# Kernel tuning notes

Measured on AMD Instinct MI355X. Metric: run time of the kernel, lower is better.

Reference implementation:

```python
import jax, jax.numpy as jnp
import numpy as np

D_MODEL = 1024
N_HEADS = 16
D_HEAD = D_MODEL // N_HEADS
EPS_LN = 1e-5
EPS_GATE = 1e-5
EPS_DEN = 1e-5


def setup_inputs() -> dict:
    key = jax.random.key(0)
    ks = jax.random.split(key, 4)
    B, T, D = 1, 2048, D_MODEL
    x = jax.random.normal(ks[0], (B, T, D), dtype=jnp.float32)
    # Linear weights scaled like torch default init (~1/sqrt(fan_in))
    s = 1.0 / np.sqrt(D)
    qkv_w = jax.random.normal(ks[1], (3 * D, D), dtype=jnp.float32) * s
    gate_w = jax.random.normal(ks[2], (D, D), dtype=jnp.float32) * s
    proj_w = jax.random.normal(ks[3], (D, D), dtype=jnp.float32) * s
    return {
        "x": x,
        "ln_g": jnp.ones((D,), jnp.float32),
        "ln_b": jnp.zeros((D,), jnp.float32),
        "qkv_w": qkv_w,
        "qkv_b": jnp.zeros((3 * D,), jnp.float32),
        "gate_w": gate_w,
        "gate_b": jnp.zeros((D,), jnp.float32),
        "proj_w": proj_w,
        "proj_b": jnp.zeros((D,), jnp.float32),
    }


def _linear(x, w, b):
    # torch nn.Linear: y = x @ W^T + b, W is (out, in)
    return jnp.einsum("btd,od->bto", x, w) + b


def reference(x, ln_g, ln_b, qkv_w, qkv_b, gate_w, gate_b, proj_w, proj_b):
    B, T, D = x.shape
    H, Dh = N_HEADS, D_HEAD

    # LayerNorm
    mu = jnp.mean(x, axis=-1, keepdims=True)
    var = jnp.mean((x - mu) ** 2, axis=-1, keepdims=True)
    x_norm = (x - mu) / jnp.sqrt(var + EPS_LN) * ln_g + ln_b

    qkv = _linear(x_norm, qkv_w, qkv_b)
    q, k, v = jnp.split(qkv, 3, axis=-1)

    # concept gate on raw x
    gate_sig = jax.nn.sigmoid(_linear(x, gate_w, gate_b))
    gate_norm = gate_sig / (jnp.mean(gate_sig, axis=-1, keepdims=True) + EPS_GATE)
    q = q * gate_norm
    k = k * gate_norm

    # (B,T,D) -> (B,H,T,Dh)
    def heads(t):
        return t.reshape(B, T, H, Dh).transpose(0, 2, 1, 3)

    q, k, v = heads(q).astype(jnp.float32), heads(k).astype(jnp.float32), heads(v).astype(jnp.float32)

    q = jax.nn.elu(q) + 1.0
    k = jax.nn.elu(k) + 1.0

    # causal linear attention via cumsum of outer products (same math as source)
    kv = jnp.einsum("bhtd,bhtm->bhtdm", k, v)        # (B,H,T,Dh,Dh)
    kv_cum = jnp.cumsum(kv, axis=2)
    out_num = jnp.einsum("bhtd,bhtdm->bhtm", q, kv_cum)
    k_cum = jnp.cumsum(k, axis=2)
    out_den = jnp.einsum("bhtd,bhtd->bht", q, k_cum)[..., None] + EPS_DEN
    out = out_num / out_den                           # (B,H,T,Dh)

    out = out.astype(x_norm.dtype).transpose(0, 2, 1, 3).reshape(B, T, D)
    return _linear(out, proj_w, proj_b)
```

## Files before the change

kernel.cpp:

```cpp
#include <hip/hip_runtime.h>
#include <hip/hip_bf16.h>
#include <math.h>

#define T_SEQ 2048
#define DM 1024
#define NH 16
#define DH 64
#define CHUNK 64
#define NCHUNK (T_SEQ / CHUNK)

typedef __hip_bfloat16 bf16;
typedef __attribute__((ext_vector_type(8))) short short8;
typedef __attribute__((ext_vector_type(4))) short short4v;
typedef __attribute__((ext_vector_type(4))) float f32x4;

static __device__ __forceinline__ short f2b_bits(float f) {
  bf16 t = __float2bfloat16(f);
  short s;
  __builtin_memcpy(&s, &t, 2);
  return s;
}
static __device__ __forceinline__ float b2f(short s) {
  unsigned int u = ((unsigned int)(unsigned short)s) << 16;
  float f;
  __builtin_memcpy(&f, &u, 4);
  return f;
}
static __device__ __forceinline__ float gelu1(float raw, float gate, float inv) {
  float x = raw * gate * inv;
  return x > 0.f ? x + 1.f : __expf(x);
}
static __device__ __forceinline__ void gload16(const void* g, void* l) {
  __builtin_amdgcn_global_load_lds((const __attribute__((address_space(1))) void*)g,
                                   (__attribute__((address_space(3))) void*)l, 16, 0, 0);
}

#define PREP_WBLOCKS (5 * DM * DM / 4 / 256)
__global__ __launch_bounds__(256) void prep_kernel(
    const float* __restrict__ x, const float* __restrict__ g,
    const float* __restrict__ b, const float* __restrict__ qkv_w,
    const float* __restrict__ gate_w, const float* __restrict__ proj_w,
    bf16* __restrict__ xn, bf16* __restrict__ xbf,
    bf16* __restrict__ wqkv, bf16* __restrict__ wgate, bf16* __restrict__ wproj,
    float* __restrict__ gate_accum) {
  const int blk = blockIdx.x;
  if (blk < T_SEQ) {
    const int row = blk;
    if (row < 8) gate_accum[row * 256 + threadIdx.x] = 0.f;
    const float* xr = x + (size_t)row * DM;
    float vals[4];
    float s = 0.f, s2 = 0.f;
#pragma unroll
    for (int i = 0; i < 4; i++) {
      float v = xr[threadIdx.x + i * 256];
      vals[i] = v;
      s += v;
      s2 += v * v;
    }
#pragma unroll
    for (int m = 1; m < 64; m <<= 1) {
      s += __shfl_xor(s, m, 64);
      s2 += __shfl_xor(s2, m, 64);
    }
    __shared__ float red[8];
    const int wid = threadIdx.x >> 6;
    if ((threadIdx.x & 63) == 0) {
      red[wid] = s;
      red[4 + wid] = s2;
    }
    __syncthreads();
    s = red[0] + red[1] + red[2] + red[3];
    s2 = red[4] + red[5] + red[6] + red[7];
    const float mean = s * (1.f / DM);
    const float var = s2 * (1.f / DM) - mean * mean;
    const float rstd = rsqrtf(var + 1e-5f);
#pragma unroll
    for (int i = 0; i < 4; i++) {
      int idx = threadIdx.x + i * 256;
      float v = (vals[i] - mean) * rstd * g[idx] + b[idx];
      xn[(size_t)row * DM + idx] = __float2bfloat16(v);
      xbf[(size_t)row * DM + idx] = __float2bfloat16(vals[i]);
    }
  } else {
    constexpr int NQ = 3 * DM * DM / 4, NS = DM * DM / 4;
    int i = (blk - T_SEQ) * 256 + threadIdx.x;
    const float* src;
    bf16* dst;
    int j;
    if (i < NQ) { src = qkv_w; dst = wqkv; j = i; }
    else if (i < NQ + NS) { src = gate_w; dst = wgate; j = i - NQ; }
    else { src = proj_w; dst = wproj; j = i - NQ - NS; }
    float4 v = ((const float4*)src)[j];
    short4v sv;
    sv.x = f2b_bits(v.x); sv.y = f2b_bits(v.y); sv.z = f2b_bits(v.z); sv.w = f2b_bits(v.w);
    *(short4v*)&dst[j * 4] = sv;
  }
}

__global__ __launch_bounds__(256) void gemm_gateqkv(
    const bf16* __restrict__ xbf, const bf16* __restrict__ xn,
    const bf16* __restrict__ wg, const bf16* __restrict__ wq,
    const float* __restrict__ gate_b, const float* __restrict__ qkv_b,
    short* __restrict__ Gb, float* __restrict__ gate_accum,
    short* __restrict__ Qb, short* __restrict__ Kb, short* __restrict__ Vb,
    short* __restrict__ VbT) {
  constexpr int K = 1024;
  __shared__ __align__(16) short As[2 * 64 * 32];
  __shared__ __align__(16) short Bs[2 * 128 * 32];

  const int tid = threadIdx.x;
  const int wid = tid >> 6, lane = tid & 63;
  const int wm = wid >> 1, wn = wid & 1;
  const int lm = lane & 15, quad = lane >> 4;

  const int nt = blockIdx.x;
  const bool isGate = nt < 8;
  const int m0 = blockIdx.y * 64;
  const int n0 = (isGate ? nt : nt - 8) * 128;
  const short* Ag = (const short*)(isGate ? xbf : xn);
  const short* Wg = (const short*)(isGate ? wg : wq);

  f32x4 zero = {0.f, 0.f, 0.f, 0.f};
  f32x4 acc[2][4];
#pragma unroll
  for (int i = 0; i < 2; i++)
#pragma unroll
    for (int j = 0; j < 4; j++) acc[i][j] = zero;

  for (int kb = 0; kb < K; kb += 64) {
    __syncthreads();
#pragma unroll
    for (int sec = 0; sec < 2; sec++) {
      {
        const int row = tid >> 2, seg = (tid & 3) * 8;
        gload16(&Ag[(size_t)(m0 + row) * K + kb + sec * 32 + seg],
                &As[sec * 2048 + wid * 512]);
      }
#pragma unroll
      for (int it = 0; it < 2; it++) {
        const int idx = it * 256 + tid;
        const int row = idx >> 2, seg = (idx & 3) * 8;
        gload16(&Wg[(size_t)(n0 + row) * K + kb + sec * 32 + seg],
                &Bs[sec * 4096 + (it * 256 + wid * 64) * 8]);
      }
    }
    __syncthreads();
#pragma unroll
    for (int sec = 0; sec < 2; sec++) {
      short8 afr[2], bfr[4];
#pragma unroll
      for (int i = 0; i < 2; i++)
        afr[i] = *(const short8*)&As[sec * 2048 + (wm * 32 + i * 16 + lm) * 32 + quad * 8];
#pragma unroll
      for (int j = 0; j < 4; j++)
        bfr[j] = *(const short8*)&Bs[sec * 4096 + (wn * 64 + j * 16 + lm) * 32 + quad * 8];
#pragma unroll
      for (int i = 0; i < 2; i++)
#pragma unroll
        for (int j = 0; j < 4; j++)
          acc[i][j] = __builtin_amdgcn_mfma_f32_16x16x32_bf16(afr[i], bfr[j], acc[i][j], 0, 0, 0);
    }
  }

  if (isGate) {
    float* red = (float*)As;
    __syncthreads();
#pragma unroll
    for (int i = 0; i < 2; i++) {
#pragma unroll
      for (int r = 0; r < 4; r++) {
        const int rowl = wm * 32 + i * 16 + quad * 4 + r;
        const int row = m0 + rowl;
        float rp = 0.f;
#pragma unroll
        for (int j = 0; j < 4; j++) {
          const int col = n0 + wn * 64 + j * 16 + lm;
          float v = acc[i][j][r] + gate_b[col];
          float sig = 1.f / (1.f + __expf(-v));
          Gb[(size_t)row * DM + col] = f2b_bits(sig);
          rp += sig;
        }
        red[rowl * 32 + wn * 16 + lm] = rp;
      }
    }
    __syncthreads();
    if (tid < 64) {
      float s = 0.f;
#pragma unroll
      for (int t2 = 0; t2 < 32; t2++) s += red[tid * 32 + t2];
      atomicAdd(&gate_accum[m0 + tid], s);
    }
  } else {
#pragma unroll
    for (int i = 0; i < 2; i++) {
      const int rbase = m0 + wm * 32 + i * 16 + quad * 4;
#pragma unroll
      for (int j = 0; j < 4; j++) {
        const int col = n0 + wn * 64 + j * 16 + lm;
        const float bval = qkv_b[col];
#pragma unroll
        for (int r = 0; r < 4; r++) {
          const int row = rbase + r;
          const short bv = f2b_bits(acc[i][j][r] + bval);
          if (col < DM) {
            const int d = col;
            Qb[((size_t)(d >> 6) * T_SEQ + row) * DH + (d & 63)] = bv;
          } else if (col < 2 * DM) {
            const int d = col - DM;
            Kb[((size_t)(d >> 6) * T_SEQ + row) * DH + (d & 63)] = bv;
          } else {
            const int d = col - 2 * DM;
            Vb[((size_t)(d >> 6) * T_SEQ + row) * DH + (d & 63)] = bv;
            VbT[((size_t)(d >> 6) * DH + (d & 63)) * T_SEQ + row] = bv;
          }
        }
      }
    }
  }
}

__global__ __launch_bounds__(256, 2) void chunk_sum_mm(const short* __restrict__ Kb,
                                                       const short* __restrict__ Gb,
                                                       const float* __restrict__ ga,
                                                       const short* __restrict__ Vb,
                                                       float* __restrict__ SkvT,
                                                       float* __restrict__ Sk) {
  constexpr int STR = 68;
  __shared__ __align__(16) float Ks2[64 * STR];
  __shared__ __align__(16) float Vs2[64 * STR];
  const int b = blockIdx.x;
  const int h = b >> 5, c = b & 31;
  const int tid = threadIdx.x;
  const int ty = tid >> 4, tx = tid & 15;
  const int d0 = ty * 4, m0 = tx * 4;
  const int t0 = c * CHUNK;
  const size_t cb = ((size_t)h * T_SEQ + t0) * DH;
#pragma unroll
  for (int p = 0; p < 4; p++) {
    int f = p * 256 + tid, row = f >> 4, seg = (f & 15) * 4;
    const int t = t0 + row;
    short4v kr = *(const short4v*)&Kb[cb + row * 64 + seg];
    short4v gr = *(const short4v*)&Gb[(size_t)t * DM + h * 64 + seg];
    short4v vr = *(const short4v*)&Vb[cb + row * 64 + seg];
    const float inv = 1.f / (ga[t] * (1.f / DM) + 1e-5f);
    f32x4 kgv, vv;
#pragma unroll
    for (int e = 0; e < 4; e++) {
      kgv[e] = gelu1(b2f(kr[e]), b2f(gr[e]), inv);
      vv[e] = b2f(vr[e]);
    }
    *(f32x4*)&Ks2[row * STR + seg] = kgv;
    *(f32x4*)&Vs2[row * STR + seg] = vv;
  }
  __syncthreads();
  float acc[4][4] = {};
#pragma unroll 4
  for (int s = 0; s < 64; s++) {
    f32x4 kf = *(const f32x4*)&Ks2[s * STR + d0];
    f32x4 vf = *(const f32x4*)&Vs2[s * STR + m0];
#pragma unroll
    for (int i = 0; i < 4; i++)
#pragma unroll
      for (int j = 0; j < 4; j++) acc[i][j] += kf[i] * vf[j];
  }
  float* outp = SkvT + (size_t)b * 4096;
#pragma unroll
  for (int i = 0; i < 4; i++)
#pragma unroll
    for (int j = 0; j < 4; j++)
      outp[(m0 + j) * 64 + (d0 + i)] = acc[i][j];
  if (tid < 64) {
    float ss = 0.f;
#pragma unroll 4
    for (int s = 0; s < 64; s++) ss += Ks2[s * STR + tid];
    Sk[b * 64 + tid] = ss;
  }
}

__global__ __launch_bounds__(256) void scan_excl(float* __restrict__ Skv,
                                                 float* __restrict__ Sk) {
  const int bid = blockIdx.x, tid = threadIdx.x;
  if (bid < 256) {
    const int id = bid * 256 + tid;
    const int h = id >> 12, e = id & 4095;
    float* base = Skv + (size_t)h * NCHUNK * 4096 + e;
    float v[NCHUNK];
#pragma unroll
    for (int c = 0; c < NCHUNK; c++) v[c] = base[(size_t)c * 4096];
    float run = 0.f;
#pragma unroll
    for (int c = 0; c < NCHUNK; c++) {
      float t = v[c];
      base[(size_t)c * 4096] = run;
      run += t;
    }
  } else {
    const int id = (bid - 256) * 256 + tid;
    const int h = id >> 6, e = id & 63;
    float* base = Sk + (size_t)h * NCHUNK * 64 + e;
    float v[NCHUNK];
#pragma unroll
    for (int c = 0; c < NCHUNK; c++) v[c] = base[c * 64];
    float run = 0.f;
#pragma unroll
    for (int c = 0; c < NCHUNK; c++) {
      float t = v[c];
      base[c * 64] = run;
      run += t;
    }
  }
}

__global__ __launch_bounds__(256, 2) void attn_mfma(const short* __restrict__ Qb,
                                                    const short* __restrict__ Kb,
                                                    const short* __restrict__ Gb,
                                                    const float* __restrict__ ga,
                                                    const short* __restrict__ VbT,
                                                    const float* __restrict__ SkvT,
                                                    const float* __restrict__ Sk,
                                                    bf16* __restrict__ O) {
  constexpr int STR = 72;
  __shared__ __align__(16) short Qs[64 * STR];
  __shared__ __align__(16) short Ks[64 * STR];
  __shared__ __align__(16) short Vt[64 * STR];
  __shared__ __align__(16) short Pt[64 * STR];
  __shared__ __align__(16) short SL[64 * STR];
  __shared__ float denp[64], invden[64], skp[64];
  const int b = blockIdx.x;
  const int h = b >> 5, c = b & 31;
  const int tid = threadIdx.x;
  const int wid = tid >> 6, lane = tid & 63;
  const int lm = lane & 15, quad = lane >> 4;
  const int t0 = c * CHUNK;
  const size_t cb = ((size_t)h * T_SEQ + t0) * DH;
  const float* Pg = SkvT + (size_t)b * 4096;

#pragma unroll
  for (int p = 0; p < 4; p++) {
    const int f = p * 256 + tid, row = f >> 4, seg = (f & 15) * 4;
    const int t = t0 + row;
    short4v qr = *(const short4v*)&Qb[cb + row * 64 + seg];
    short4v kr = *(const short4v*)&Kb[cb + row * 64 + seg];
    short4v gr = *(const short4v*)&Gb[(size_t)t * DM + h * 64 + seg];
    short4v vtr = *(const short4v*)&VbT[((size_t)h * DH + row) * T_SEQ + t0 + seg];
    f32x4 pr = *(const f32x4*)&Pg[row * 64 + seg];
    const float inv = 1.f / (ga[t] * (1.f / DM) + 1e-5f);
    short4v qs, ks, ps;
#pragma unroll
    for (int e = 0; e < 4; e++) {
      qs[e] = f2b_bits(gelu1(b2f(qr[e]), b2f(gr[e]), inv));
      ks[e] = f2b_bits(gelu1(b2f(kr[e]), b2f(gr[e]), inv));
      ps[e] = f2b_bits(pr[e]);
    }
    *(short4v*)&Qs[row * STR + seg] = qs;
    *(short4v*)&Ks[row * STR + seg] = ks;
    *(short4v*)&Vt[row * STR + seg] = vtr;
    *(short4v*)&Pt[row * STR + seg] = ps;
  }
  if (tid < 64) skp[tid] = Sk[b * 64 + tid];
  __syncthreads();

  f32x4 zero = {0.f, 0.f, 0.f, 0.f};
  short8 aq[2];
#pragma unroll
  for (int ks = 0; ks < 2; ks++)
    aq[ks] = *(const short8*)&Qs[(wid * 16 + lm) * STR + ks * 32 + quad * 8];
  f32x4 accs[4];
#pragma unroll
  for (int j = 0; j < 4; j++) accs[j] = zero;
#pragma unroll
  for (int j = 0; j < 4; j++)
#pragma unroll
    for (int ks = 0; ks < 2; ks++) {
      short8 bk = *(const short8*)&Ks[(j * 16 + lm) * STR + ks * 32 + quad * 8];
      accs[j] = __builtin_amdgcn_mfma_f32_16x16x32_bf16(aq[ks], bk, accs[j], 0, 0, 0);
    }
  float rowpart[4] = {0.f, 0.f, 0.f, 0.f};
#pragma unroll
  for (int j = 0; j < 4; j++) {
    const int s = j * 16 + lm;
#pragma unroll
    for (int r = 0; r < 4; r++) {
      const int t = wid * 16 + quad * 4 + r;
      float v = (s <= t) ? accs[j][r] : 0.f;
      accs[j][r] = v;
      rowpart[r] += v;
    }
  }
#pragma unroll
  for (int msk = 1; msk < 16; msk <<= 1)
#pragma unroll
    for (int r = 0; r < 4; r++) rowpart[r] += __shfl_xor(rowpart[r], msk, 64);
  if (lm == 0)
#pragma unroll
    for (int r = 0; r < 4; r++) denp[wid * 16 + quad * 4 + r] = rowpart[r];
#pragma unroll
  for (int j = 0; j < 4; j++)
#pragma unroll
    for (int r = 0; r < 4; r++)
      SL[(wid * 16 + quad * 4 + r) * STR + j * 16 + lm] = f2b_bits(accs[j][r]);

  f32x4 acco[4];
#pragma unroll
  for (int j = 0; j < 4; j++) acco[j] = zero;
  short8 ap[2];
#pragma unroll
  for (int ks = 0; ks < 2; ks++)
    ap[ks] = *(const short8*)&Pt[(wid * 16 + lm) * STR + ks * 32 + quad * 8];
#pragma unroll
  for (int j = 0; j < 4; j++)
#pragma unroll
    for (int ks = 0; ks < 2; ks++) {
      short8 bq = *(const short8*)&Qs[(j * 16 + lm) * STR + ks * 32 + quad * 8];
      acco[j] = __builtin_amdgcn_mfma_f32_16x16x32_bf16(ap[ks], bq, acco[j], 0, 0, 0);
    }
  __syncthreads();

  if (tid < 64) {
    float s = 1e-5f + denp[tid];
    for (int d = 0; d < 64; d++) s += b2f(Qs[tid * STR + d]) * skp[d];
    invden[tid] = 1.f / s;
  }

  short8 av[2];
#pragma unroll
  for (int ks = 0; ks < 2; ks++)
    av[ks] = *(const short8*)&Vt[(wid * 16 + lm) * STR + ks * 32 + quad * 8];
#pragma unroll
  for (int j = 0; j < 4; j++)
#pragma unroll
    for (int ks = 0; ks < 2; ks++) {
      short8 bs = *(const short8*)&SL[(j * 16 + lm) * STR + ks * 32 + quad * 8];
      acco[j] = __builtin_amdgcn_mfma_f32_16x16x32_bf16(av[ks], bs, acco[j], 0, 0, 0);
    }
  __syncthreads();

#pragma unroll
  for (int j = 0; j < 4; j++) {
    const int t = j * 16 + lm;
    const float idv = invden[t];
    short4v ov;
#pragma unroll
    for (int r = 0; r < 4; r++) ov[r] = f2b_bits(acco[j][r] * idv);
    *(short4v*)&((short*)O)[(size_t)(t0 + t) * DM + h * 64 + wid * 16 + quad * 4] = ov;
  }
}

__global__ __launch_bounds__(256) void gemm_proj(const bf16* __restrict__ A,
                                                 const bf16* __restrict__ W,
                                                 const float* __restrict__ bias,
                                                 float* __restrict__ Cout) {
  constexpr int K = 1024;
  __shared__ __align__(16) short As[2 * 64 * 32];
  __shared__ __align__(16) short Bs[2 * 64 * 32];

  const int tid = threadIdx.x;
  const int wid = tid >> 6, lane = tid & 63;
  const int wm = wid >> 1, wn = wid & 1;
  const int lm = lane & 15, quad = lane >> 4;

  const int n0 = blockIdx.x * 64;
  const int m0 = blockIdx.y * 64;
  const short* Ag = (const short*)A;
  const short* Wg = (const short*)W;

  f32x4 zero = {0.f, 0.f, 0.f, 0.f};
  f32x4 acc[2][2];
#pragma unroll
  for (int i = 0; i < 2; i++)
#pragma unroll
    for (int j = 0; j < 2; j++) acc[i][j] = zero;

  for (int kb = 0; kb < K; kb += 64) {
    __syncthreads();
#pragma unroll
    for (int sec = 0; sec < 2; sec++) {
      const int row = tid >> 2, seg = (tid & 3) * 8;
      gload16(&Ag[(size_t)(m0 + row) * K + kb + sec * 32 + seg],
              &As[sec * 2048 + wid * 512]);
      gload16(&Wg[(size_t)(n0 + row) * K + kb + sec * 32 + seg],
              &Bs[sec * 2048 + wid * 512]);
    }
    __syncthreads();
#pragma unroll
    for (int sec = 0; sec < 2; sec++) {
      short8 afr[2], bfr[2];
#pragma unroll
      for (int i = 0; i < 2; i++)
        afr[i] = *(const short8*)&As[sec * 2048 + (wm * 32 + i * 16 + lm) * 32 + quad * 8];
#pragma unroll
      for (int j = 0; j < 2; j++)
        bfr[j] = *(const short8*)&Bs[sec * 2048 + (wn * 32 + j * 16 + lm) * 32 + quad * 8];
#pragma unroll
      for (int i = 0; i < 2; i++)
#pragma unroll
        for (int j = 0; j < 2; j++)
          acc[i][j] = __builtin_amdgcn_mfma_f32_16x16x32_bf16(afr[i], bfr[j], acc[i][j], 0, 0, 0);
    }
  }
#pragma unroll
  for (int i = 0; i < 2; i++) {
    const int rbase = m0 + wm * 32 + i * 16 + quad * 4;
#pragma unroll
    for (int j = 0; j < 2; j++) {
      const int col = n0 + wn * 32 + j * 16 + lm;
      const float bval = bias[col];
#pragma unroll
      for (int r = 0; r < 4; r++)
        Cout[(size_t)(rbase + r) * DM + col] = acc[i][j][r] + bval;
    }
  }
}

extern "C" void kernel_launch(void* const* d_in, const int* in_sizes, int n_in,
                              void* d_out, int out_size, void* d_ws, size_t ws_size,
                              hipStream_t stream) {
  (void)in_sizes; (void)n_in; (void)out_size; (void)ws_size;
  const float* x      = (const float*)d_in[0];
  const float* ln_g   = (const float*)d_in[1];
  const float* ln_b   = (const float*)d_in[2];
  const float* qkv_w  = (const float*)d_in[3];
  const float* qkv_b  = (const float*)d_in[4];
  const float* gate_w = (const float*)d_in[5];
  const float* gate_b = (const float*)d_in[6];
  const float* proj_w = (const float*)d_in[7];
  const float* proj_b = (const float*)d_in[8];
  float* out = (float*)d_out;

  char* ws = (char*)d_ws;
  size_t off = 0;
  auto alloc = [&](size_t bytes) {
    void* p = ws + off;
    off += (bytes + 255) & ~(size_t)255;
    return p;
  };
  bf16*  xn       = (bf16*)alloc((size_t)T_SEQ * DM * 2);
  bf16*  xbf      = (bf16*)alloc((size_t)T_SEQ * DM * 2);
  bf16*  wqkv     = (bf16*)alloc((size_t)3 * DM * DM * 2);
  bf16*  wgate    = (bf16*)alloc((size_t)DM * DM * 2);
  bf16*  wproj    = (bf16*)alloc((size_t)DM * DM * 2);
  short* Gb       = (short*)alloc((size_t)T_SEQ * DM * 2);
  float* gate_accum = (float*)alloc((size_t)T_SEQ * 4);
  short* Qb       = (short*)alloc((size_t)T_SEQ * DM * 2);
  short* Kb       = (short*)alloc((size_t)T_SEQ * DM * 2);
  short* Vb       = (short*)alloc((size_t)T_SEQ * DM * 2);
  short* VbT      = (short*)alloc((size_t)T_SEQ * DM * 2);
  bf16*  Obuf     = (bf16*)alloc((size_t)T_SEQ * DM * 2);
  float* SkvT     = (float*)alloc((size_t)NH * NCHUNK * 4096 * 4);
  float* Sk       = (float*)alloc((size_t)NH * NCHUNK * 64 * 4);

  prep_kernel<<<T_SEQ + PREP_WBLOCKS, 256, 0, stream>>>(
      x, ln_g, ln_b, qkv_w, gate_w, proj_w, xn, xbf, wqkv, wgate, wproj, gate_accum);
  gemm_gateqkv<<<dim3(32, 32), 256, 0, stream>>>(xbf, xn, wgate, wqkv, gate_b, qkv_b,
                                                 Gb, gate_accum, Qb, Kb, Vb, VbT);
  chunk_sum_mm<<<NH * NCHUNK, 256, 0, stream>>>(Kb, Gb, gate_accum, Vb, SkvT, Sk);
  scan_excl<<<260, 256, 0, stream>>>(SkvT, Sk);
  attn_mfma<<<NH * NCHUNK, 256, 0, stream>>>(Qb, Kb, Gb, gate_accum, VbT, SkvT, Sk, Obuf);
  gemm_proj<<<dim3(16, 32), 256, 0, stream>>>(Obuf, wproj, proj_b, out);
}
```

Before: 164.0 us.

## Double-buffer LDS tiles in gate/QKV and projection GEMMs

Both GEMM kernels now keep two LDS buffers and issue the global-to-LDS loads for the next K-step before running the MFMAs on the current one. This cuts one barrier per iteration and is meant to overlap global load latency with matrix compute. The cost is twice the shared memory per block, which may lower occupancy. Correctness depends on gload16 completing before the single remaining barrier.

```diff
diff --git a/kernel.cpp b/kernel.cpp
--- a/kernel.cpp
+++ b/kernel.cpp
@@ -105,8 +105,8 @@
     short* __restrict__ Qb, short* __restrict__ Kb, short* __restrict__ Vb,
     short* __restrict__ VbT) {
   constexpr int K = 1024;
-  __shared__ __align__(16) short As[2 * 64 * 32];
-  __shared__ __align__(16) short Bs[2 * 128 * 32];
+  __shared__ __align__(16) short As[2 * 2 * 64 * 32];
+  __shared__ __align__(16) short Bs[2 * 2 * 128 * 32];
 
   const int tid = threadIdx.x;
   const int wid = tid >> 6, lane = tid & 63;
@@ -127,38 +127,53 @@
 #pragma unroll
     for (int j = 0; j < 4; j++) acc[i][j] = zero;
 
-  for (int kb = 0; kb < K; kb += 64) {
-    __syncthreads();
+  const int arow = tid >> 2, aseg = (tid & 3) * 8;
+
+  auto stage = [&](int db, int kb) {
 #pragma unroll
     for (int sec = 0; sec < 2; sec++) {
-      {
-        const int row = tid >> 2, seg = (tid & 3) * 8;
-        gload16(&Ag[(size_t)(m0 + row) * K + kb + sec * 32 + seg],
-                &As[sec * 2048 + wid * 512]);
-      }
+      gload16(&Ag[(size_t)(m0 + arow) * K + kb + sec * 32 + aseg],
+              &As[db * 4096 + sec * 2048 + wid * 512]);
 #pragma unroll
       for (int it = 0; it < 2; it++) {
         const int idx = it * 256 + tid;
         const int row = idx >> 2, seg = (idx & 3) * 8;
         gload16(&Wg[(size_t)(n0 + row) * K + kb + sec * 32 + seg],
-                &Bs[sec * 4096 + (it * 256 + wid * 64) * 8]);
+                &Bs[db * 8192 + sec * 4096 + (it * 256 + wid * 64) * 8]);
       }
     }
-    __syncthreads();
+  };
+  auto compute = [&](int db) {
 #pragma unroll
     for (int sec = 0; sec < 2; sec++) {
       short8 afr[2], bfr[4];
 #pragma unroll
       for (int i = 0; i < 2; i++)
-        afr[i] = *(const short8*)&As[sec * 2048 + (wm * 32 + i * 16 + lm) * 32 + quad * 8];
+        afr[i] = *(const short8*)&As[db * 4096 + sec * 2048 +
+                                     (wm * 32 + i * 16 + lm) * 32 + quad * 8];
 #pragma unroll
       for (int j = 0; j < 4; j++)
-        bfr[j] = *(const short8*)&Bs[sec * 4096 + (wn * 64 + j * 16 + lm) * 32 + quad * 8];
+        bfr[j] = *(const short8*)&Bs[db * 8192 + sec * 4096 +
+                                     (wn * 64 + j * 16 + lm) * 32 + quad * 8];
 #pragma unroll
       for (int i = 0; i < 2; i++)
 #pragma unroll
         for (int j = 0; j < 4; j++)
           acc[i][j] = __builtin_amdgcn_mfma_f32_16x16x32_bf16(afr[i], bfr[j], acc[i][j], 0, 0, 0);
+    }
+  };
+
+  stage(0, 0);
+  __syncthreads();
+  int cur = 0;
+  for (int kb = 0; kb < K; kb += 64) {
+    if (kb + 64 < K) {
+      stage(cur ^ 1, kb + 64);
+      compute(cur);
+      __syncthreads();
+      cur ^= 1;
+    } else {
+      compute(cur);
     }
   }
 
@@ -451,8 +466,8 @@
                                                  const float* __restrict__ bias,
                                                  float* __restrict__ Cout) {
   constexpr int K = 1024;
-  __shared__ __align__(16) short As[2 * 64 * 32];
-  __shared__ __align__(16) short Bs[2 * 64 * 32];
+  __shared__ __align__(16) short As[2 * 2 * 64 * 32];
+  __shared__ __align__(16) short Bs[2 * 2 * 64 * 32];
 
   const int tid = threadIdx.x;
   const int wid = tid >> 6, lane = tid & 63;
@@ -471,33 +486,51 @@
 #pragma unroll
     for (int j = 0; j < 2; j++) acc[i][j] = zero;
 
-  for (int kb = 0; kb < K; kb += 64) {
-    __syncthreads();
+  const int arow = tid >> 2, aseg = (tid & 3) * 8;
+
+  auto stage = [&](int db, int kb) {
 #pragma unroll
     for (int sec = 0; sec < 2; sec++) {
-      const int row = tid >> 2, seg = (tid & 3) * 8;
-      gload16(&Ag[(size_t)(m0 + row) * K + kb + sec * 32 + seg],
-              &As[sec * 2048 + wid * 512]);
-      gload16(&Wg[(size_t)(n0 + row) * K + kb + sec * 32 + seg],
-              &Bs[sec * 2048 + wid * 512]);
-    }
-    __syncthreads();
+      gload16(&Ag[(size_t)(m0 + arow) * K + kb + sec * 32 + aseg],
+              &As[db * 4096 + sec * 2048 + wid * 512]);
+      gload16(&Wg[(size_t)(n0 + arow) * K + kb + sec * 32 + aseg],
+              &Bs[db * 4096 + sec * 2048 + wid * 512]);
+    }
+  };
+  auto compute = [&](int db) {
 #pragma unroll
     for (int sec = 0; sec < 2; sec++) {
       short8 afr[2], bfr[2];
 #pragma unroll
       for (int i = 0; i < 2; i++)
-        afr[i] = *(const short8*)&As[sec * 2048 + (wm * 32 + i * 16 + lm) * 32 + quad * 8];
+        afr[i] = *(const short8*)&As[db * 4096 + sec * 2048 +
+                                     (wm * 32 + i * 16 + lm) * 32 + quad * 8];
 #pragma unroll
       for (int j = 0; j < 2; j++)
-        bfr[j] = *(const short8*)&Bs[sec * 2048 + (wn * 32 + j * 16 + lm) * 32 + quad * 8];
+        bfr[j] = *(const short8*)&Bs[db * 4096 + sec * 2048 +
+                                     (wn * 32 + j * 16 + lm) * 32 + quad * 8];
 #pragma unroll
       for (int i = 0; i < 2; i++)
 #pragma unroll
         for (int j = 0; j < 2; j++)
           acc[i][j] = __builtin_amdgcn_mfma_f32_16x16x32_bf16(afr[i], bfr[j], acc[i][j], 0, 0, 0);
     }
-  }
+  };
+
+  stage(0, 0);
+  __syncthreads();
+  int cur = 0;
+  for (int kb = 0; kb < K; kb += 64) {
+    if (kb + 64 < K) {
+      stage(cur ^ 1, kb + 64);
+      compute(cur);
+      __syncthreads();
+      cur ^= 1;
+    } else {
+      compute(cur);
+    }
+  }
+
 #pragma unroll
   for (int i = 0; i < 2; i++) {
     const int rbase = m0 + wm * 32 + i * 16 + quad * 4;
```

Result: slower. 170.7 us (+4.1%).

## Triple-buffer gate/QKV GEMM loads and parallelize denominator reduction

Applied to the files above, without the earlier changes.

Restructures the gate/QKV GEMM main loop into a three-stage shared-memory ring of 32-wide K tiles. Loads are issued two tiles ahead and gated by vmcnt waits with a single barrier per step, so global loads overlap MFMA work instead of alternating load and compute phases. Separately, the attention denominator dot product is split across all 256 threads, four per row, and combined with shuffles rather than done serially by 64 threads. The pipeline uses more LDS, which may reduce occupancy, and relies on hand-written waitcnt counts being correct.

```diff
diff --git a/kernel.cpp b/kernel.cpp
--- a/kernel.cpp
+++ b/kernel.cpp
@@ -105,8 +105,9 @@
     short* __restrict__ Qb, short* __restrict__ Kb, short* __restrict__ Vb,
     short* __restrict__ VbT) {
   constexpr int K = 1024;
-  __shared__ __align__(16) short As[2 * 64 * 32];
-  __shared__ __align__(16) short Bs[2 * 128 * 32];
+  constexpr int NT = K / 32;
+  __shared__ __align__(16) short As[3 * 64 * 32];
+  __shared__ __align__(16) short Bs[3 * 128 * 32];
 
   const int tid = threadIdx.x;
   const int wid = tid >> 6, lane = tid & 63;
@@ -127,39 +128,47 @@
 #pragma unroll
     for (int j = 0; j < 4; j++) acc[i][j] = zero;
 
-  for (int kb = 0; kb < K; kb += 64) {
-    __syncthreads();
-#pragma unroll
-    for (int sec = 0; sec < 2; sec++) {
-      {
-        const int row = tid >> 2, seg = (tid & 3) * 8;
-        gload16(&Ag[(size_t)(m0 + row) * K + kb + sec * 32 + seg],
-                &As[sec * 2048 + wid * 512]);
-      }
-#pragma unroll
-      for (int it = 0; it < 2; it++) {
-        const int idx = it * 256 + tid;
-        const int row = idx >> 2, seg = (idx & 3) * 8;
-        gload16(&Wg[(size_t)(n0 + row) * K + kb + sec * 32 + seg],
-                &Bs[sec * 4096 + (it * 256 + wid * 64) * 8]);
-      }
-    }
-    __syncthreads();
-#pragma unroll
-    for (int sec = 0; sec < 2; sec++) {
-      short8 afr[2], bfr[4];
-#pragma unroll
-      for (int i = 0; i < 2; i++)
-        afr[i] = *(const short8*)&As[sec * 2048 + (wm * 32 + i * 16 + lm) * 32 + quad * 8];
+  const int arow = tid >> 2, aseg = (tid & 3) * 8;
+
+  auto stage = [&](int db, int t) {
+    const int kb = t * 32;
+    gload16(&Ag[(size_t)(m0 + arow) * K + kb + aseg], &As[db * 2048 + wid * 512]);
+#pragma unroll
+    for (int it = 0; it < 2; it++) {
+      const int idx = it * 256 + tid;
+      const int row = idx >> 2, seg = (idx & 3) * 8;
+      gload16(&Wg[(size_t)(n0 + row) * K + kb + seg],
+              &Bs[db * 4096 + it * 2048 + wid * 512]);
+    }
+  };
+
+  stage(0, 0);
+  stage(1, 1);
+  int db = 0;
+  for (int t = 0; t < NT; t++) {
+    if (t < NT - 1)
+      asm volatile("s_waitcnt vmcnt(3)" ::: "memory");
+    else
+      asm volatile("s_waitcnt vmcnt(0)" ::: "memory");
+    __builtin_amdgcn_s_barrier();
+    __builtin_amdgcn_sched_barrier(0);
+    short8 afr[2], bfr[4];
+#pragma unroll
+    for (int i = 0; i < 2; i++)
+      afr[i] = *(const short8*)&As[db * 2048 + (wm * 32 + i * 16 + lm) * 32 + quad * 8];
+#pragma unroll
+    for (int j = 0; j < 4; j++)
+      bfr[j] = *(const short8*)&Bs[db * 4096 + (wn * 64 + j * 16 + lm) * 32 + quad * 8];
+    if (t + 2 < NT) {
+      const int dbn = db >= 1 ? db - 1 : 2;
+      stage(dbn, t + 2);
+    }
+#pragma unroll
+    for (int i = 0; i < 2; i++)
 #pragma unroll
       for (int j = 0; j < 4; j++)
-        bfr[j] = *(const short8*)&Bs[sec * 4096 + (wn * 64 + j * 16 + lm) * 32 + quad * 8];
-#pragma unroll
-      for (int i = 0; i < 2; i++)
-#pragma unroll
-        for (int j = 0; j < 4; j++)
-          acc[i][j] = __builtin_amdgcn_mfma_f32_16x16x32_bf16(afr[i], bfr[j], acc[i][j], 0, 0, 0);
-    }
+        acc[i][j] = __builtin_amdgcn_mfma_f32_16x16x32_bf16(afr[i], bfr[j], acc[i][j], 0, 0, 0);
+    db = db == 2 ? 0 : db + 1;
   }
 
   if (isGate) {
@@ -416,10 +425,17 @@
     }
   __syncthreads();
 
-  if (tid < 64) {
-    float s = 1e-5f + denp[tid];
-    for (int d = 0; d < 64; d++) s += b2f(Qs[tid * STR + d]) * skp[d];
-    invden[tid] = 1.f / s;
+  {
+    const int row = tid >> 2, part = tid & 3;
+    float s = 0.f;
+#pragma unroll
+    for (int dd = 0; dd < 16; dd++) {
+      const int d = part * 16 + dd;
+      s += b2f(Qs[row * STR + d]) * skp[d];
+    }
+    s += __shfl_xor(s, 1, 64);
+    s += __shfl_xor(s, 2, 64);
+    if (part == 0) invden[row] = 1.f / (1e-5f + denp[row] + s);
   }
 
   short8 av[2];
```

New measurement: 164.9 us. No clear change (+0.6%).
